# Kernel optimization log

Measured on AMD Instinct MI355X. Metric: run time of the kernel, lower is better.

## Reference

```python
import jax, jax.numpy as jnp
import numpy as np

VOCAB = 50257
EMB = 2048
HID = 2048  # must equal EMB per module's hidden init
TAGS = 50
SEQ = 1024


def setup_inputs() -> dict:
    key = jax.random.key(0)
    ks = jax.random.split(key, 8)
    s = 0.02
    return {
        "sequence": jax.random.randint(ks[0], (SEQ,), 0, VOCAB),
        "emb": jax.random.normal(ks[1], (VOCAB, EMB), jnp.float32) * s,
        "W_ih": jax.random.normal(ks[2], (4 * HID, EMB), jnp.float32) * s,
        "W_hh": jax.random.normal(ks[3], (4 * HID, HID), jnp.float32) * s,
        "b_ih": jax.random.normal(ks[4], (4 * HID,), jnp.float32) * s,
        "b_hh": jax.random.normal(ks[5], (4 * HID,), jnp.float32) * s,
        "W_tag": jax.random.normal(ks[6], (TAGS, HID), jnp.float32) * s,
        "b_tag": jax.random.normal(ks[7], (TAGS,), jnp.float32) * s,
    }


def reference(sequence, emb, W_ih, W_hh, b_ih, b_hh, W_tag, b_tag):
    H = W_hh.shape[1]
    # Pre-gather embeddings for all timesteps: [S, EMB]
    xs = emb[sequence]
    # Pre-compute input-side gate pre-activations for all steps: [S, 4H]
    x_gates = xs @ W_ih.T + b_ih + b_hh

    def step(carry, xg):
        h, c = carry
        gates = xg + h @ W_hh.T  # [4H]
        i, f, g, o = jnp.split(gates, 4)
        i = jax.nn.sigmoid(i)
        f = jax.nn.sigmoid(f)
        g = jnp.tanh(g)
        o = jax.nn.sigmoid(o)
        c = f * c + i * g
        h = o * jnp.tanh(c)
        return (h, c), None

    h0 = jnp.zeros((H,), emb.dtype)
    c0 = jnp.zeros((H,), emb.dtype)
    (h, _), _ = jax.lax.scan(step, (h0, c0), x_gates)

    tag_space = h @ W_tag.T + b_tag  # [TAGS]
    return jax.nn.log_softmax(tag_space, axis=0)
```

## Files before the change

kernel.cpp:

```cpp
#include <hip/hip_runtime.h>

#define SEQL 1024
#define EMB  2048
#define HID  2048
#define G4   8192
#define NTAG 50
#define NWG  256

typedef _Float16 h2v __attribute__((ext_vector_type(2)));
typedef _Float16 h4v __attribute__((ext_vector_type(4)));

#if __has_builtin(__builtin_amdgcn_fdot2)
#define DOT2(a, b, c) __builtin_amdgcn_fdot2((a), (b), (c), false)
#else
#define DOT2(a, b, c) ((c) + (float)(a).x * (float)(b).x + (float)(a).y * (float)(b).y)
#endif
#define SH2(v, i, j) __builtin_shufflevector((v), (v), (i), (j))

__global__ __launch_bounds__(256) void gemm_xgates(
    const int* __restrict__ seq, const float* __restrict__ emb,
    const float* __restrict__ Wih, const float* __restrict__ bih,
    const float* __restrict__ bhh, float* __restrict__ xg,
    unsigned int* __restrict__ hslot, int* __restrict__ flags)
{
    if (blockIdx.x == 0 && blockIdx.y == 0) {
        for (int i = threadIdx.x; i < 2 * HID; i += 256) hslot[i] = 0;
        if (threadIdx.x < NWG) flags[threadIdx.x] = 0;
    }

    constexpr int BM = 128, BN = 128, BK = 32;
    __shared__ float As[BK][BM + 4];
    __shared__ float Bs[BK][BN + 4];
    __shared__ int   srow[BM];

    const int tid = threadIdx.x;
    const int bn = blockIdx.x, bm = blockIdx.y;

    if (tid < BM) srow[tid] = seq[bm * BM + tid];
    __syncthreads();

    const int tx = tid & 15, ty = tid >> 4;
    const int c4 = tid & 7;
    const int r0 = tid >> 3;

    float acc[8][8] = {};

    for (int k0 = 0; k0 < EMB; k0 += BK) {
        #pragma unroll
        for (int i = 0; i < 4; ++i) {
            const int r = r0 + 32 * i;
            float4 av = *(const float4*)(emb + (size_t)srow[r] * EMB + k0 + 4 * c4);
            As[4*c4+0][r] = av.x; As[4*c4+1][r] = av.y;
            As[4*c4+2][r] = av.z; As[4*c4+3][r] = av.w;
            float4 bv = *(const float4*)(Wih + (size_t)(bn * BN + r) * EMB + k0 + 4 * c4);
            Bs[4*c4+0][r] = bv.x; Bs[4*c4+1][r] = bv.y;
            Bs[4*c4+2][r] = bv.z; Bs[4*c4+3][r] = bv.w;
        }
        __syncthreads();
        #pragma unroll
        for (int kk = 0; kk < BK; ++kk) {
            float a[8], b[8];
            *(float4*)&a[0] = *(const float4*)&As[kk][8*ty];
            *(float4*)&a[4] = *(const float4*)&As[kk][8*ty+4];
            *(float4*)&b[0] = *(const float4*)&Bs[kk][8*tx];
            *(float4*)&b[4] = *(const float4*)&Bs[kk][8*tx+4];
            #pragma unroll
            for (int i = 0; i < 8; ++i)
                #pragma unroll
                for (int j = 0; j < 8; ++j)
                    acc[i][j] += a[i] * b[j];
        }
        __syncthreads();
    }

    const int gm = bm * BM + 8 * ty;
    const int gn = bn * BN + 8 * tx;
    float bb[8];
    #pragma unroll
    for (int j = 0; j < 8; ++j) bb[j] = bih[gn + j] + bhh[gn + j];
    #pragma unroll
    for (int i = 0; i < 8; ++i) {
        float4 o0, o1;
        o0.x = acc[i][0] + bb[0]; o0.y = acc[i][1] + bb[1];
        o0.z = acc[i][2] + bb[2]; o0.w = acc[i][3] + bb[3];
        o1.x = acc[i][4] + bb[4]; o1.y = acc[i][5] + bb[5];
        o1.z = acc[i][6] + bb[6]; o1.w = acc[i][7] + bb[7];
        *(float4*)(xg + (size_t)(gm + i) * G4 + gn)     = o0;
        *(float4*)(xg + (size_t)(gm + i) * G4 + gn + 4) = o1;
    }
}

__device__ __forceinline__ uint4 ld_u4_l3(const void* p) {
    uint4 r;
    asm volatile("global_load_dwordx4 %0, %1, off sc0 sc1\n\ts_waitcnt vmcnt(0)"
                 : "=v"(r) : "v"(p) : "memory");
    return r;
}
__device__ __forceinline__ int ld_i32_l3(const void* p) {
    int r;
    asm volatile("global_load_dword %0, %1, off sc0 sc1\n\ts_waitcnt vmcnt(0)"
                 : "=v"(r) : "v"(p) : "memory");
    return r;
}
__device__ __forceinline__ float ld_f32_l3(const void* p) {
    float r;
    asm volatile("global_load_dword %0, %1, off sc0 sc1\n\ts_waitcnt vmcnt(0)"
                 : "=v"(r) : "v"(p) : "memory");
    return r;
}
__device__ __forceinline__ void st_u32_l3(void* p, unsigned int v) {
    asm volatile("global_store_dword %0, %1, off sc0 sc1"
                 :: "v"(p), "v"(v) : "memory");
}
__device__ __forceinline__ void st_f32_l3(void* p, float v) {
    asm volatile("global_store_dword %0, %1, off sc0 sc1"
                 :: "v"(p), "v"(v) : "memory");
}
__device__ __forceinline__ void wait_vm0() {
    asm volatile("s_waitcnt vmcnt(0)" ::: "memory");
}

__device__ __forceinline__ float sigm_(float x) { return 1.0f / (1.0f + __expf(-x)); }
__device__ __forceinline__ float tanh_(float x) {
    float e = __expf(2.0f * x);
    return (e - 1.0f) / (e + 1.0f);
}

__global__ __launch_bounds__(512, 1) void lstm_recur(
    const float* __restrict__ Whh, const float* __restrict__ xg,
    const float* __restrict__ Wtag, const float* __restrict__ btag,
    unsigned int* __restrict__ hslot, float* __restrict__ tags,
    float* __restrict__ out, int* __restrict__ flags)
{
    __shared__ __align__(16) ushort wf16[8][4][HID];
    __shared__ __align__(16) ushort shh16[HID];
    __shared__ float sh_red[8];

    const int tid = threadIdx.x;
    const int wv  = tid >> 6;
    const int l   = tid & 63;
    const int bid = blockIdx.x;
    const int j   = 8 * bid + wv;

    #pragma unroll
    for (int q = 0; q < 4; ++q) {
        const float* wr = Whh + (size_t)(q * HID + j) * HID;
        #pragma unroll
        for (int i = 0; i < 4; ++i) {
            const int c8 = l + 64 * i;
            float4 va = *(const float4*)(wr + 8 * c8);
            float4 vb = *(const float4*)(wr + 8 * c8 + 4);
            h4v wa = {(_Float16)va.x, (_Float16)va.y, (_Float16)va.z, (_Float16)va.w};
            h4v wb = {(_Float16)vb.x, (_Float16)vb.y, (_Float16)vb.z, (_Float16)vb.w};
            *(h4v*)&wf16[wv][q][8 * c8]     = wa;
            *(h4v*)&wf16[wv][q][8 * c8 + 4] = wb;
        }
    }

    auto poll_stage = [&](int target, int parity) {
        const unsigned int* base = hslot + parity * HID + 4 * tid;
        const ushort tgt = (ushort)target;
        uint4 d;
        for (;;) {
            d = ld_u4_l3(base);
            if ((((ushort)(d.x >> 16)) == tgt) & (((ushort)(d.y >> 16)) == tgt) &
                (((ushort)(d.z >> 16)) == tgt) & (((ushort)(d.w >> 16)) == tgt))
                break;
        }
        ushort4 hh = {(ushort)d.x, (ushort)d.y, (ushort)d.z, (ushort)d.w};
        *(ushort4*)&shh16[4 * tid] = hh;
        __syncthreads();
    };

    float cst = 0.0f;
    float xg0 = xg[j], xg1 = xg[j + HID], xg2 = xg[j + 2 * HID], xg3 = xg[j + 3 * HID];

    for (int t = 0; t < SEQL; ++t) {
        if (t > 0) poll_stage(t, (t - 1) & 1);
        else       __syncthreads();

        const int tn = (t + 1 < SEQL) ? t + 1 : t;
        const size_t xb = (size_t)tn * G4 + j;
        const float nx0 = xg[xb];
        const float nx1 = xg[xb + HID];
        const float nx2 = xg[xb + 2 * HID];
        const float nx3 = xg[xb + 3 * HID];

        float s0 = 0.f, s1 = 0.f, s2 = 0.f, s3 = 0.f;
        if (t > 0) {
            #pragma unroll
            for (int r = 0; r < 4; ++r) {
                const int kc = 8 * (l + 64 * r);
                h4v ha = *(const h4v*)&shh16[kc];
                h4v hb = *(const h4v*)&shh16[kc + 4];
                h2v h0 = SH2(ha, 0, 1), h1 = SH2(ha, 2, 3);
                h2v h2 = SH2(hb, 0, 1), h3 = SH2(hb, 2, 3);
                h4v w;
                w = *(const h4v*)&wf16[wv][0][kc];
                s0 = DOT2(SH2(w,0,1), h0, s0); s0 = DOT2(SH2(w,2,3), h1, s0);
                w = *(const h4v*)&wf16[wv][0][kc + 4];
                s0 = DOT2(SH2(w,0,1), h2, s0); s0 = DOT2(SH2(w,2,3), h3, s0);
                w = *(const h4v*)&wf16[wv][1][kc];
                s1 = DOT2(SH2(w,0,1), h0, s1); s1 = DOT2(SH2(w,2,3), h1, s1);
                w = *(const h4v*)&wf16[wv][1][kc + 4];
                s1 = DOT2(SH2(w,0,1), h2, s1); s1 = DOT2(SH2(w,2,3), h3, s1);
                w = *(const h4v*)&wf16[wv][2][kc];
                s2 = DOT2(SH2(w,0,1), h0, s2); s2 = DOT2(SH2(w,2,3), h1, s2);
                w = *(const h4v*)&wf16[wv][2][kc + 4];
                s2 = DOT2(SH2(w,0,1), h2, s2); s2 = DOT2(SH2(w,2,3), h3, s2);
                w = *(const h4v*)&wf16[wv][3][kc];
                s3 = DOT2(SH2(w,0,1), h0, s3); s3 = DOT2(SH2(w,2,3), h1, s3);
                w = *(const h4v*)&wf16[wv][3][kc + 4];
                s3 = DOT2(SH2(w,0,1), h2, s3); s3 = DOT2(SH2(w,2,3), h3, s3);
            }
        }
        #pragma unroll
        for (int m = 1; m < 64; m <<= 1) {
            s0 += __shfl_xor(s0, m);
            s1 += __shfl_xor(s1, m);
            s2 += __shfl_xor(s2, m);
            s3 += __shfl_xor(s3, m);
        }
        const float gi = sigm_(s0 + xg0);
        const float gf = sigm_(s1 + xg1);
        const float gg = tanh_(s2 + xg2);
        const float go = sigm_(s3 + xg3);
        cst = gf * cst + gi * gg;
        const float h = go * tanh_(cst);

        if (l == 0) {
            _Float16 hf = (_Float16)h;
            unsigned int d = ((unsigned int)(ushort)(t + 1) << 16)
                           | (unsigned int)__builtin_bit_cast(ushort, hf);
            st_u32_l3(hslot + (t & 1) * HID + j, d);
        }

        xg0 = nx0; xg1 = nx1; xg2 = nx2; xg3 = nx3;
    }

    poll_stage(SEQL, (SEQL - 1) & 1);
    if (bid < NTAG) {
        h4v hv4 = *(const h4v*)&shh16[4 * tid];
        float4 w4 = *(const float4*)(Wtag + (size_t)bid * HID + 4 * tid);
        float part = w4.x * (float)hv4.x + w4.y * (float)hv4.y
                   + w4.z * (float)hv4.z + w4.w * (float)hv4.w;
        #pragma unroll
        for (int m = 1; m < 64; m <<= 1) part += __shfl_xor(part, m);
        if (l == 0) sh_red[wv] = part;
    }
    __syncthreads();
    if (bid < NTAG && tid == 0) {
        float s = 0.f;
        #pragma unroll
        for (int i = 0; i < 8; ++i) s += sh_red[i];
        st_f32_l3(tags + bid, s + btag[bid]);
    }
    wait_vm0();
    __syncthreads();
    if (tid == 0) st_u32_l3((unsigned int*)(flags + bid), 1u);

    if (bid == 0) {
        for (;;) {
            int ok = 1;
            if (tid < NTAG) ok = (ld_i32_l3(flags + tid) >= 1);
            if (__syncthreads_and(ok)) break;
            __builtin_amdgcn_s_sleep(1);
        }
        if (tid < 64) {
            float v = (tid < NTAG) ? ld_f32_l3(tags + tid) : -3.0e38f;
            float mx = v;
            #pragma unroll
            for (int m = 1; m < 64; m <<= 1) mx = fmaxf(mx, __shfl_xor(mx, m));
            float e = (tid < NTAG) ? __expf(v - mx) : 0.f;
            float se = e;
            #pragma unroll
            for (int m = 1; m < 64; m <<= 1) se += __shfl_xor(se, m);
            if (tid < NTAG) out[tid] = v - mx - __logf(se);
        }
    }
}

extern "C" void kernel_launch(void* const* d_in, const int* in_sizes, int n_in,
                              void* d_out, int out_size, void* d_ws, size_t ws_size,
                              hipStream_t stream)
{
    const int*   seq  = (const int*)d_in[0];
    const float* emb  = (const float*)d_in[1];
    const float* Wih  = (const float*)d_in[2];
    const float* Whh  = (const float*)d_in[3];
    const float* bih  = (const float*)d_in[4];
    const float* bhh  = (const float*)d_in[5];
    const float* Wtag = (const float*)d_in[6];
    const float* btag = (const float*)d_in[7];
    float* out = (float*)d_out;

    float* xg = (float*)d_ws;
    unsigned int* hslot = (unsigned int*)(xg + (size_t)SEQL * G4);
    float* tags  = (float*)(hslot + 2 * HID);
    int*   flags = (int*)(tags + 64);

    dim3 g1(G4 / 128, SEQL / 128);
    gemm_xgates<<<g1, 256, 0, stream>>>(seq, emb, Wih, bih, bhh, xg, hslot, flags);

    void* args[] = {(void*)&Whh, (void*)&xg, (void*)&Wtag, (void*)&btag,
                    (void*)&hslot, (void*)&tags, (void*)&out, (void*)&flags};
    hipLaunchCooperativeKernel((void*)lstm_recur, dim3(NWG), dim3(512),
                               args, 0, stream);
}
```

Measured before the change: 3.368 ms.

## Use bf16 MFMA for input-gate GEMM with swizzled LDS tiles

Rewrites the x-gates GEMM to convert emb and W_ih tiles to bf16 on the fly and compute with MFMA 16x16x32 bf16 instructions instead of scalar FP32 FMAs. LDS tiles are stored row-major with an XOR swizzle to avoid bank conflicts, and BK grows to 64. This targets the compute cost of the 1024x8192x2048 GEMM but lowers input precision to bf16, which may affect accuracy over the long recurrence. The output store also becomes scalar rather than float4.

```diff
diff --git a/kernel.cpp b/kernel.cpp
--- a/kernel.cpp
+++ b/kernel.cpp
@@ -9,6 +9,8 @@
 
 typedef _Float16 h2v __attribute__((ext_vector_type(2)));
 typedef _Float16 h4v __attribute__((ext_vector_type(4)));
+typedef __attribute__((ext_vector_type(8))) short bf16x8;
+typedef __attribute__((ext_vector_type(4))) float f32x4;
 
 #if __has_builtin(__builtin_amdgcn_fdot2)
 #define DOT2(a, b, c) __builtin_amdgcn_fdot2((a), (b), (c), false)
@@ -16,6 +18,12 @@
 #define DOT2(a, b, c) ((c) + (float)(a).x * (float)(b).x + (float)(a).y * (float)(b).y)
 #endif
 #define SH2(v, i, j) __builtin_shufflevector((v), (v), (i), (j))
+
+__device__ __forceinline__ ushort f2bf_rne(float f) {
+    unsigned u = __float_as_uint(f);
+    unsigned r = (u + 0x7fffu + ((u >> 16) & 1u)) >> 16;
+    return (ushort)r;
+}
 
 __global__ __launch_bounds__(256) void gemm_xgates(
     const int* __restrict__ seq, const float* __restrict__ emb,
@@ -28,10 +36,10 @@
         if (threadIdx.x < NWG) flags[threadIdx.x] = 0;
     }
 
-    constexpr int BM = 128, BN = 128, BK = 32;
-    __shared__ float As[BK][BM + 4];
-    __shared__ float Bs[BK][BN + 4];
-    __shared__ int   srow[BM];
+    constexpr int BM = 128, BN = 128, BK = 64;
+    __shared__ __align__(16) ushort Al[BM][BK];
+    __shared__ __align__(16) ushort Bl[BN][BK];
+    __shared__ int srow[BM];
 
     const int tid = threadIdx.x;
     const int bn = blockIdx.x, bm = blockIdx.y;
@@ -39,54 +47,79 @@
     if (tid < BM) srow[tid] = seq[bm * BM + tid];
     __syncthreads();
 
-    const int tx = tid & 15, ty = tid >> 4;
-    const int c4 = tid & 7;
-    const int r0 = tid >> 3;
-
-    float acc[8][8] = {};
+    const int lane = tid & 63;
+    const int wave = tid >> 6;
+    const int wm = (wave >> 1) * 64;
+    const int wn = (wave & 1) * 64;
+    const int srw = tid >> 1;
+    const int skh = (tid & 1) * 32;
+    const int cb  = skh >> 3;
+
+    f32x4 acc[4][4] = {};
 
     for (int k0 = 0; k0 < EMB; k0 += BK) {
-        #pragma unroll
-        for (int i = 0; i < 4; ++i) {
-            const int r = r0 + 32 * i;
-            float4 av = *(const float4*)(emb + (size_t)srow[r] * EMB + k0 + 4 * c4);
-            As[4*c4+0][r] = av.x; As[4*c4+1][r] = av.y;
-            As[4*c4+2][r] = av.z; As[4*c4+3][r] = av.w;
-            float4 bv = *(const float4*)(Wih + (size_t)(bn * BN + r) * EMB + k0 + 4 * c4);
-            Bs[4*c4+0][r] = bv.x; Bs[4*c4+1][r] = bv.y;
-            Bs[4*c4+2][r] = bv.z; Bs[4*c4+3][r] = bv.w;
+        const float* ap = emb + (size_t)srow[srw] * EMB + k0 + skh;
+        const float* bp = Wih + (size_t)(bn * BN + srw) * EMB + k0 + skh;
+        #pragma unroll
+        for (int c = 0; c < 4; ++c) {
+            float4 a0 = *(const float4*)(ap + 8 * c);
+            float4 a1 = *(const float4*)(ap + 8 * c + 4);
+            bf16x8 av;
+            av[0] = (short)f2bf_rne(a0.x); av[1] = (short)f2bf_rne(a0.y);
+            av[2] = (short)f2bf_rne(a0.z); av[3] = (short)f2bf_rne(a0.w);
+            av[4] = (short)f2bf_rne(a1.x); av[5] = (short)f2bf_rne(a1.y);
+            av[6] = (short)f2bf_rne(a1.z); av[7] = (short)f2bf_rne(a1.w);
+            *(bf16x8*)&Al[srw][8 * ((cb + c) ^ (srw & 7))] = av;
+
+            float4 b0 = *(const float4*)(bp + 8 * c);
+            float4 b1 = *(const float4*)(bp + 8 * c + 4);
+            bf16x8 bv;
+            bv[0] = (short)f2bf_rne(b0.x); bv[1] = (short)f2bf_rne(b0.y);
+            bv[2] = (short)f2bf_rne(b0.z); bv[3] = (short)f2bf_rne(b0.w);
+            bv[4] = (short)f2bf_rne(b1.x); bv[5] = (short)f2bf_rne(b1.y);
+            bv[6] = (short)f2bf_rne(b1.z); bv[7] = (short)f2bf_rne(b1.w);
+            *(bf16x8*)&Bl[srw][8 * ((cb + c) ^ (srw & 7))] = bv;
         }
         __syncthreads();
-        #pragma unroll
-        for (int kk = 0; kk < BK; ++kk) {
-            float a[8], b[8];
-            *(float4*)&a[0] = *(const float4*)&As[kk][8*ty];
-            *(float4*)&a[4] = *(const float4*)&As[kk][8*ty+4];
-            *(float4*)&b[0] = *(const float4*)&Bs[kk][8*tx];
-            *(float4*)&b[4] = *(const float4*)&Bs[kk][8*tx+4];
-            #pragma unroll
-            for (int i = 0; i < 8; ++i)
+
+        const int kg = lane >> 4;
+        #pragma unroll
+        for (int ks = 0; ks < 2; ++ks) {
+            bf16x8 af[4], bfr[4];
+            #pragma unroll
+            for (int f = 0; f < 4; ++f) {
+                const int ra = wm + f * 16 + (lane & 15);
+                af[f]  = *(const bf16x8*)&Al[ra][8 * ((ks * 4 + kg) ^ (ra & 7))];
+                const int rb = wn + f * 16 + (lane & 15);
+                bfr[f] = *(const bf16x8*)&Bl[rb][8 * ((ks * 4 + kg) ^ (rb & 7))];
+            }
+            #pragma unroll
+            for (int i = 0; i < 4; ++i)
                 #pragma unroll
-                for (int j = 0; j < 8; ++j)
-                    acc[i][j] += a[i] * b[j];
+                for (int j2 = 0; j2 < 4; ++j2)
+                    acc[i][j2] = __builtin_amdgcn_mfma_f32_16x16x32_bf16(
+                        af[i], bfr[j2], acc[i][j2], 0, 0, 0);
         }
         __syncthreads();
     }
 
-    const int gm = bm * BM + 8 * ty;
-    const int gn = bn * BN + 8 * tx;
-    float bb[8];
+    float bb[4];
     #pragma unroll
-    for (int j = 0; j < 8; ++j) bb[j] = bih[gn + j] + bhh[gn + j];
+    for (int j2 = 0; j2 < 4; ++j2) {
+        const int col = bn * BN + wn + j2 * 16 + (lane & 15);
+        bb[j2] = bih[col] + bhh[col];
+    }
     #pragma unroll
-    for (int i = 0; i < 8; ++i) {
-        float4 o0, o1;
-        o0.x = acc[i][0] + bb[0]; o0.y = acc[i][1] + bb[1];
-        o0.z = acc[i][2] + bb[2]; o0.w = acc[i][3] + bb[3];
-        o1.x = acc[i][4] + bb[4]; o1.y = acc[i][5] + bb[5];
-        o1.z = acc[i][6] + bb[6]; o1.w = acc[i][7] + bb[7];
-        *(float4*)(xg + (size_t)(gm + i) * G4 + gn)     = o0;
-        *(float4*)(xg + (size_t)(gm + i) * G4 + gn + 4) = o1;
+    for (int i = 0; i < 4; ++i) {
+        #pragma unroll
+        for (int e = 0; e < 4; ++e) {
+            const int row = bm * BM + wm + i * 16 + (lane >> 4) * 4 + e;
+            #pragma unroll
+            for (int j2 = 0; j2 < 4; ++j2) {
+                const int col = bn * BN + wn + j2 * 16 + (lane & 15);
+                xg[(size_t)row * G4 + col] = acc[i][j2][e] + bb[j2];
+            }
+        }
     }
 }
 
```

Result: faster. 2.834 ms (-15.9%).
